# Kernel optimization log

Hardware: AMD Instinct MI355X
Metric: run time of the kernel (lower is better)

Reference implementation:

```python
import jax, jax.numpy as jnp
import numpy as np

NUM_HEADS = 8
DIM_IN = 512
DIM_OUT = 512


def setup_inputs() -> dict:
    key = jax.random.key(0)
    k1, k2, k3, k4, k5, k6 = jax.random.split(key, 6)
    B, T, J, C = 8, 243, 17, DIM_IN
    H = NUM_HEADS
    x = jax.random.normal(k1, (B, T, J, C), dtype=jnp.float32)
    # external attention map over temporal axis per joint: [B,H,J,T,T]
    att_map = jax.random.uniform(k2, (B, H, J, T, T), dtype=jnp.float32)
    weight = jax.random.uniform(k3, (1,), dtype=jnp.float32)
    # learned params (torch Linear stored here as [in,out] so y = x @ W)
    W_qkv = jax.random.normal(k4, (C, 3 * C), dtype=jnp.float32) * (C ** -0.5)
    W_proj = jax.random.normal(k5, (C, DIM_OUT), dtype=jnp.float32) * (C ** -0.5)
    b_proj = jax.random.normal(k6, (DIM_OUT,), dtype=jnp.float32) * 0.02
    return {"x": x, "att_map": att_map, "weight": weight,
            "W_qkv": W_qkv, "W_proj": W_proj, "b_proj": b_proj}


def reference(x, att_map, weight, W_qkv, W_proj, b_proj):
    B, T, J, C = x.shape
    H = NUM_HEADS
    hd = C // H
    scale = hd ** -0.5
    qkv = (x @ W_qkv).reshape(B, T, J, 3, H, hd)
    # permute(3,0,4,1,2,5) then transpose(2,3) -> [3,B,H,J,T,hd]
    qkv = jnp.transpose(qkv, (3, 0, 4, 2, 1, 5))
    q, k, v = qkv[0], qkv[1], qkv[2]
    attn = jax.nn.softmax(jnp.einsum('bhjtd,bhjsd->bhjts', q, k) * scale, axis=-1)
    attn = weight * attn + (1.0 - weight) * att_map  # dropout is identity (p=0 / eval)
    out = jnp.einsum('bhjts,bhjsd->bhjtd', attn, v)  # [B,H,J,T,hd]
    out = jnp.transpose(out, (0, 3, 2, 1, 4)).reshape(B, T, J, H * hd)
    return out @ W_proj + b_proj
```

## Files before the change

kernel.cpp:

```cpp
#include <hip/hip_runtime.h>
#include <cstddef>
#include <cstdint>

#define NHEADS 8
#define TT 243
#define JJ 17
#define BB 8
#define CC 512
#define HD 64
#define MROWS 33048
#define TJ 4131
#define HJ 136

typedef __attribute__((ext_vector_type(8))) short bf16x8;
typedef __attribute__((ext_vector_type(4))) float f32x4;

__device__ __forceinline__ unsigned short f2bf(float f) {
    unsigned u = __float_as_uint(f);
    unsigned r = (u + 0x7fff + ((u >> 16) & 1)) >> 16;
    return (unsigned short)r;
}
__device__ __forceinline__ float b2f(unsigned short u) {
    return __uint_as_float(((unsigned)u) << 16);
}
__device__ __forceinline__ void async16(const void* g, void* l) {
    __builtin_amdgcn_global_load_lds(
        (const __attribute__((address_space(1))) void*)g,
        (__attribute__((address_space(3))) void*)l, 16, 0, 0);
}

__global__ __launch_bounds__(256) void convert_x(
    const float* __restrict__ in, unsigned short* __restrict__ out, int n4)
{
    for (int i = blockIdx.x * 256 + threadIdx.x; i < n4; i += gridDim.x * 256) {
        const float4 v = *(const float4*)(in + (size_t)i * 4);
        ushort4 o;
        o.x = f2bf(v.x); o.y = f2bf(v.y); o.z = f2bf(v.z); o.w = f2bf(v.w);
        *(ushort4*)(out + (size_t)i * 4) = o;
    }
}

__global__ __launch_bounds__(256) void transpose_w(
    const float* __restrict__ src, unsigned short* __restrict__ dst, int N)
{
    __shared__ unsigned short tile[64][65];
    const int tid = threadIdx.x;
    const int c = tid & 63, r4 = tid >> 6;
    const int n0 = blockIdx.x << 6, k0 = blockIdx.y << 6;
    #pragma unroll
    for (int p = 0; p < 16; ++p) {
        const int r = (p << 2) + r4;
        tile[r][c] = f2bf(src[(size_t)(k0 + r) * N + n0 + c]);
    }
    __syncthreads();
    #pragma unroll
    for (int p = 0; p < 16; ++p) {
        const int rr = (p << 2) + r4;
        dst[(size_t)(n0 + rr) * 512 + k0 + c] = tile[c][rr];
    }
}

__global__ __launch_bounds__(256) void gemm_qkv(
    const unsigned short* __restrict__ xb, const unsigned short* __restrict__ wt,
    unsigned short* __restrict__ qb, unsigned short* __restrict__ kb,
    unsigned short* __restrict__ vb)
{
    __shared__ __align__(16) char smem[32768];
    char* const A0 = smem;
    char* const A1 = smem + 8192;
    char* const B0 = smem + 16384;
    char* const B1 = smem + 24576;

    const int tid = threadIdx.x;
    const int wave = tid >> 6, lane = tid & 63;
    const int m0 = blockIdx.y << 7, n0 = blockIdx.x << 7;
    const int wr = wave >> 1, wc = wave & 1;

    f32x4 acc[4][4];
    #pragma unroll
    for (int i = 0; i < 4; ++i)
        #pragma unroll
        for (int j = 0; j < 4; ++j) acc[i][j] = (f32x4){0.f, 0.f, 0.f, 0.f};

    const int srow = lane >> 2;
    const int sbyte = (lane & 3) << 4;
    const int arow0 = (wave << 5) + srow;
    const int arow1 = arow0 + 16;
    const size_t am0 = (size_t)min(m0 + arow0, MROWS - 1);
    const size_t am1 = (size_t)min(m0 + arow1, MROWS - 1);
    const char* xbb = (const char*)xb;
    const char* wtb = (const char*)wt;

#define STAGEQ(Ad, Bd, k0) do { \
    async16(xbb + (am0 * 512 + (k0)) * 2 + sbyte, (Ad) + ((wave << 5) << 6)); \
    async16(xbb + (am1 * 512 + (k0)) * 2 + sbyte, (Ad) + (((wave << 5) + 16) << 6)); \
    async16(wtb + ((size_t)(n0 + arow0) * 512 + (k0)) * 2 + sbyte, (Bd) + ((wave << 5) << 6)); \
    async16(wtb + ((size_t)(n0 + arow1) * 512 + (k0)) * 2 + sbyte, (Bd) + (((wave << 5) + 16) << 6)); \
} while (0)

#define COMPUTEQ(Ap, Bp) do { \
    bf16x8 af[4], bfr[4]; \
    _Pragma("unroll") \
    for (int i = 0; i < 4; ++i) \
        af[i] = *(const bf16x8*)((const unsigned short*)(Ap) + \
            ((wr << 6) + (i << 4) + (lane & 15)) * 32 + ((lane >> 4) << 3)); \
    _Pragma("unroll") \
    for (int j = 0; j < 4; ++j) \
        bfr[j] = *(const bf16x8*)((const unsigned short*)(Bp) + \
            ((wc << 6) + (j << 4) + (lane & 15)) * 32 + ((lane >> 4) << 3)); \
    _Pragma("unroll") \
    for (int i = 0; i < 4; ++i) \
        _Pragma("unroll") \
        for (int j = 0; j < 4; ++j) \
            acc[i][j] = __builtin_amdgcn_mfma_f32_16x16x32_bf16(af[i], bfr[j], acc[i][j], 0, 0, 0); \
} while (0)

    STAGEQ(A0, B0, 0);
    __syncthreads();
    #pragma unroll
    for (int t = 0; t < 16; t += 2) {
        STAGEQ(A1, B1, (t + 1) << 5);
        COMPUTEQ(A0, B0);
        __syncthreads();
        if (t + 2 < 16) STAGEQ(A0, B0, (t + 2) << 5);
        COMPUTEQ(A1, B1);
        __syncthreads();
    }
#undef STAGEQ
#undef COMPUTEQ

    unsigned short (*Cq)[16][72] = (unsigned short (*)[16][72])smem;

    const int nw = n0 + (wc << 6);
    const int which = nw >> 9;
    const int h = (nw >> 6) & 7;
    unsigned short* const dst = which == 0 ? qb : (which == 1 ? kb : vb);
    #pragma unroll
    for (int i = 0; i < 4; ++i) {
        #pragma unroll
        for (int j = 0; j < 4; ++j)
            #pragma unroll
            for (int r = 0; r < 4; ++r)
                Cq[wave][((lane >> 4) << 2) + r][(j << 4) + (lane & 15)] = f2bf(acc[i][j][r]);
        #pragma unroll
        for (int qq = 0; qq < 4; ++qq) {
            const int rr = (qq << 2) + (lane >> 4);
            const int ch = lane & 15;
            const ushort4 val = *(const ushort4*)&Cq[wave][rr][ch << 2];
            const int m = m0 + (wr << 6) + (i << 4) + rr;
            if (m < MROWS) {
                const int b = m / TJ; const int rm = m - b * TJ;
                const int t = rm / JJ; const int jj = rm - t * JJ;
                const size_t base = (((size_t)((b * NHEADS + h) * JJ + jj) * TT + t) << 6) + (ch << 2);
                *(ushort4*)(dst + base) = val;
            }
        }
    }
}

__global__ __launch_bounds__(256) void vtrans(
    const unsigned short* __restrict__ vb, unsigned short* __restrict__ vt)
{
    __shared__ unsigned short TL[64 * 264];
    const int tid = threadIdx.x;
    const int bhj = blockIdx.x;
    const unsigned short* src = vb + (size_t)bhj * TT * HD;

    {
        const int d = tid >> 2, qq = tid & 3;
        *(ushort4*)(TL + d * 264 + 240 + (qq << 2)) = make_ushort4(0, 0, 0, 0);
    }
    __syncthreads();
    #pragma unroll
    for (int p = 0; p < 16; ++p) {
        const int idxq = tid + (p << 8);
        const int t = idxq >> 4;
        if (t < TT) {
            const int d0 = (idxq & 15) << 2;
            const ushort4 u = *(const ushort4*)(src + t * HD + d0);
            TL[(d0 + 0) * 264 + t] = u.x;
            TL[(d0 + 1) * 264 + t] = u.y;
            TL[(d0 + 2) * 264 + t] = u.z;
            TL[(d0 + 3) * 264 + t] = u.w;
        }
    }
    __syncthreads();
    unsigned short* dst = vt + ((size_t)bhj << 14);
    #pragma unroll
    for (int p = 0; p < 8; ++p) {
        const int cw = tid + (p << 8);
        const int d = cw >> 5, c = cw & 31;
        const ushort4 a = *(const ushort4*)(TL + d * 264 + (c << 3));
        const ushort4 bq = *(const ushort4*)(TL + d * 264 + (c << 3) + 4);
        *(ushort4*)(dst + (d << 8) + (c << 3)) = a;
        *(ushort4*)(dst + (d << 8) + (c << 3) + 4) = bq;
    }
}

__global__ __launch_bounds__(256, 4) void attn_mfma(
    const unsigned short* __restrict__ qb, const unsigned short* __restrict__ kb,
    const unsigned short* __restrict__ vt, const float* __restrict__ att,
    const float* __restrict__ wptr, unsigned short* __restrict__ ob)
{
    __shared__ unsigned short ST[64 * 264];

    const int tid = threadIdx.x;
    const int wave = tid >> 6, lane = tid & 63;
    const int tile = blockIdx.x & 3, bhj = blockIdx.x >> 2;
    const int row0 = tile << 6;

    const unsigned short* q = qb + (size_t)bhj * TT * HD;
    const unsigned short* k = kb + (size_t)bhj * TT * HD;
    const float* am = att + (size_t)bhj * TT * TT;
    const float w = wptr[0];

    const int lm = lane & 15, lk = lane >> 4;
    bf16x8 qf[4][2];
    #pragma unroll
    for (int mi = 0; mi < 4; ++mi) {
        const int r = min(row0 + (mi << 4) + lm, TT - 1);
        #pragma unroll
        for (int kb2 = 0; kb2 < 2; ++kb2)
            qf[mi][kb2] = *(const bf16x8*)(q + r * HD + (kb2 << 5) + (lk << 3));
    }
    f32x4 acc[4][4];
    #pragma unroll
    for (int mi = 0; mi < 4; ++mi)
        #pragma unroll
        for (int nj = 0; nj < 4; ++nj) acc[mi][nj] = (f32x4){0.f, 0.f, 0.f, 0.f};
    #pragma unroll
    for (int kb2 = 0; kb2 < 2; ++kb2) {
        bf16x8 kf[4];
        #pragma unroll
        for (int nj = 0; nj < 4; ++nj) {
            const int s = min((wave << 6) + (nj << 4) + lm, TT - 1);
            kf[nj] = *(const bf16x8*)(k + s * HD + (kb2 << 5) + (lk << 3));
        }
        #pragma unroll
        for (int mi = 0; mi < 4; ++mi)
            #pragma unroll
            for (int nj = 0; nj < 4; ++nj)
                acc[mi][nj] = __builtin_amdgcn_mfma_f32_16x16x32_bf16(qf[mi][kb2], kf[nj], acc[mi][nj], 0, 0, 0);
    }
    #pragma unroll
    for (int mi = 0; mi < 4; ++mi)
        #pragma unroll
        for (int nj = 0; nj < 4; ++nj)
            #pragma unroll
            for (int r = 0; r < 4; ++r) {
                const int m = (mi << 4) + (lk << 2) + r;
                const int s = (wave << 6) + (nj << 4) + lm;
                ST[m * 264 + s] = f2bf(acc[mi][nj][r] * 0.125f);
            }
    __syncthreads();

    {
        const int row = tid >> 2, part = tid & 3;
        const int trow = row0 + row;
        unsigned short* strow = ST + row * 264;
        if (trow < TT) {
            const float* amr = am + (size_t)trow * TT;

            float areg[15][4];
            #pragma unroll
            for (int i = 0; i < 15; ++i) {
                const int s0 = (part << 2) + (i << 4);
                areg[i][0] = amr[s0 + 0];
                areg[i][1] = amr[s0 + 1];
                areg[i][2] = amr[s0 + 2];
                areg[i][3] = amr[s0 + 3];
            }
            float at0 = 0.f, at1 = 0.f, at2 = 0.f;
            if (part == 0) { at0 = amr[240]; at1 = amr[241]; at2 = amr[242]; }

            float mx = -1e30f;
            #pragma unroll
            for (int i = 0; i < 15; ++i) {
                const ushort4 u = *(const ushort4*)(strow + (part << 2) + (i << 4));
                mx = fmaxf(fmaxf(fmaxf(fmaxf(mx, b2f(u.x)), b2f(u.y)), b2f(u.z)), b2f(u.w));
            }
            if (part == 0)
                for (int s = 240; s < TT; ++s) mx = fmaxf(mx, b2f(strow[s]));
            mx = fmaxf(mx, __shfl_xor(mx, 1));
            mx = fmaxf(mx, __shfl_xor(mx, 2));
            float l = 0.f;
            #pragma unroll
            for (int i = 0; i < 15; ++i) {
                const int s0 = (part << 2) + (i << 4);
                const ushort4 u = *(const ushort4*)(strow + s0);
                const float e0 = __expf(b2f(u.x) - mx), e1 = __expf(b2f(u.y) - mx);
                const float e2 = __expf(b2f(u.z) - mx), e3 = __expf(b2f(u.w) - mx);
                l += (e0 + e1) + (e2 + e3);
                ushort4 o;
                o.x = f2bf(e0); o.y = f2bf(e1); o.z = f2bf(e2); o.w = f2bf(e3);
                *(ushort4*)(strow + s0) = o;
            }
            if (part == 0)
                for (int s = 240; s < TT; ++s) {
                    const float e = __expf(b2f(strow[s]) - mx);
                    l += e; strow[s] = f2bf(e);
                }
            l += __shfl_xor(l, 1);
            l += __shfl_xor(l, 2);
            const float sw = w / l, aw = 1.f - w;
            #pragma unroll
            for (int i = 0; i < 15; ++i) {
                const int s0 = (part << 2) + (i << 4);
                const ushort4 u = *(const ushort4*)(strow + s0);
                ushort4 o;
                o.x = f2bf(b2f(u.x) * sw + aw * areg[i][0]);
                o.y = f2bf(b2f(u.y) * sw + aw * areg[i][1]);
                o.z = f2bf(b2f(u.z) * sw + aw * areg[i][2]);
                o.w = f2bf(b2f(u.w) * sw + aw * areg[i][3]);
                *(ushort4*)(strow + s0) = o;
            }
            if (part == 0) {
                strow[240] = f2bf(b2f(strow[240]) * sw + aw * at0);
                strow[241] = f2bf(b2f(strow[241]) * sw + aw * at1);
                strow[242] = f2bf(b2f(strow[242]) * sw + aw * at2);
                for (int s = TT; s < 256; ++s) strow[s] = 0;
            }
        } else {
            #pragma unroll
            for (int i = 0; i < 16; ++i)
                *(ushort4*)(strow + (part << 2) + (i << 4)) = make_ushort4(0, 0, 0, 0);
        }
    }
    __syncthreads();

    f32x4 oacc[4];
    #pragma unroll
    for (int nj = 0; nj < 4; ++nj) oacc[nj] = (f32x4){0.f, 0.f, 0.f, 0.f};
    const unsigned short* strow3 = ST + ((wave << 4) + lm) * 264;
    const unsigned short* vtg = vt + ((size_t)bhj << 14);
    #pragma unroll 2
    for (int kb8 = 0; kb8 < 8; ++kb8) {
        const bf16x8 pf = *(const bf16x8*)(strow3 + (kb8 << 5) + (lk << 3));
        #pragma unroll
        for (int nj = 0; nj < 4; ++nj) {
            const int d = (nj << 4) + lm;
            const int chunk = (kb8 << 2) + lk;
            const bf16x8 vf = *(const bf16x8*)(vtg + (d << 8) + (chunk << 3));
            oacc[nj] = __builtin_amdgcn_mfma_f32_16x16x32_bf16(pf, vf, oacc[nj], 0, 0, 0);
        }
    }

    const int b = bhj / HJ;
    const int hj = bhj - b * HJ;
    const int h = hj / JJ;
    const int j = hj - h * JJ;
    #pragma unroll
    for (int r = 0; r < 4; ++r) {
        const int t = row0 + (wave << 4) + (lk << 2) + r;
        if (t < TT) {
            unsigned short* orow = ob + (((size_t)((b * TT + t) * JJ + j)) << 9) + (h << 6);
            #pragma unroll
            for (int nj = 0; nj < 4; ++nj)
                orow[(nj << 4) + lm] = f2bf(oacc[nj][r]);
        }
    }
}

__global__ __launch_bounds__(256) void gemm_proj(
    const unsigned short* __restrict__ obb, const unsigned short* __restrict__ wt,
    const float* __restrict__ bias, float* __restrict__ out)
{
    __shared__ __align__(16) char smem[32768];
    char* const A0 = smem;
    char* const A1 = smem + 8192;
    char* const B0 = smem + 16384;
    char* const B1 = smem + 24576;

    const int tid = threadIdx.x;
    const int wave = tid >> 6, lane = tid & 63;
    const int m0 = blockIdx.y << 7, n0 = blockIdx.x << 7;
    const int wr = wave >> 1, wc = wave & 1;

    f32x4 acc[4][4];
    #pragma unroll
    for (int i = 0; i < 4; ++i)
        #pragma unroll
        for (int j = 0; j < 4; ++j) acc[i][j] = (f32x4){0.f, 0.f, 0.f, 0.f};

    const int srow = lane >> 2;
    const int sbyte = (lane & 3) << 4;
    const int arow0 = (wave << 5) + srow;
    const int arow1 = arow0 + 16;
    const size_t am0 = (size_t)min(m0 + arow0, MROWS - 1);
    const size_t am1 = (size_t)min(m0 + arow1, MROWS - 1);
    const char* ab = (const char*)obb;
    const char* wtb = (const char*)wt;

#define STAGEP(Ad, Bd, k0) do { \
    async16(ab + (am0 * 512 + (k0)) * 2 + sbyte, (Ad) + ((wave << 5) << 6)); \
    async16(ab + (am1 * 512 + (k0)) * 2 + sbyte, (Ad) + (((wave << 5) + 16) << 6)); \
    async16(wtb + ((size_t)(n0 + arow0) * 512 + (k0)) * 2 + sbyte, (Bd) + ((wave << 5) << 6)); \
    async16(wtb + ((size_t)(n0 + arow1) * 512 + (k0)) * 2 + sbyte, (Bd) + (((wave << 5) + 16) << 6)); \
} while (0)

#define COMPUTEP(Ap, Bp) do { \
    bf16x8 af[4], bfr[4]; \
    _Pragma("unroll") \
    for (int i = 0; i < 4; ++i) \
        af[i] = *(const bf16x8*)((const unsigned short*)(Ap) + \
            ((wr << 6) + (i << 4) + (lane & 15)) * 32 + ((lane >> 4) << 3)); \
    _Pragma("unroll") \
    for (int j = 0; j < 4; ++j) \
        bfr[j] = *(const bf16x8*)((const unsigned short*)(Bp) + \
            ((wc << 6) + (j << 4) + (lane & 15)) * 32 + ((lane >> 4) << 3)); \
    _Pragma("unroll") \
    for (int i = 0; i < 4; ++i) \
        _Pragma("unroll") \
        for (int j = 0; j < 4; ++j) \
            acc[i][j] = __builtin_amdgcn_mfma_f32_16x16x32_bf16(af[i], bfr[j], acc[i][j], 0, 0, 0); \
} while (0)

    STAGEP(A0, B0, 0);
    __syncthreads();
    #pragma unroll
    for (int t = 0; t < 16; t += 2) {
        STAGEP(A1, B1, (t + 1) << 5);
        COMPUTEP(A0, B0);
        __syncthreads();
        if (t + 2 < 16) STAGEP(A0, B0, (t + 2) << 5);
        COMPUTEP(A1, B1);
        __syncthreads();
    }
#undef STAGEP
#undef COMPUTEP

    float (*Cp)[16][68] = (float (*)[16][68])smem;

    const int ch0 = lane & 15;
    const float4 bvec = *(const float4*)&bias[n0 + (wc << 6) + (ch0 << 2)];
    #pragma unroll
    for (int i = 0; i < 4; ++i) {
        #pragma unroll
        for (int j = 0; j < 4; ++j)
            #pragma unroll
            for (int r = 0; r < 4; ++r)
                Cp[wave][((lane >> 4) << 2) + r][(j << 4) + (lane & 15)] = acc[i][j][r];
        #pragma unroll
        for (int qq = 0; qq < 4; ++qq) {
            const int rr = (qq << 2) + (lane >> 4);
            const int ch = lane & 15;
            float4 val = *(const float4*)&Cp[wave][rr][ch << 2];
            const int m = m0 + (wr << 6) + (i << 4) + rr;
            if (m < MROWS) {
                val.x += bvec.x; val.y += bvec.y; val.z += bvec.z; val.w += bvec.w;
                *(float4*)(out + (size_t)m * 512 + n0 + (wc << 6) + (ch << 2)) = val;
            }
        }
    }
}

extern "C" void kernel_launch(void* const* d_in, const int* in_sizes, int n_in,
                              void* d_out, int out_size, void* d_ws, size_t ws_size,
                              hipStream_t stream)
{
    const float* x    = (const float*)d_in[0];
    const float* att  = (const float*)d_in[1];
    const float* wgt  = (const float*)d_in[2];
    const float* Wqkv = (const float*)d_in[3];
    const float* Wp   = (const float*)d_in[4];
    const float* bp   = (const float*)d_in[5];
    float* out = (float*)d_out;

    const size_t SZ = (size_t)MROWS * 512;
    unsigned short* xb    = (unsigned short*)d_ws;
    unsigned short* wqkvt = xb + SZ;
    unsigned short* wpt   = wqkvt + (size_t)1536 * 512;
    unsigned short* qb    = wpt + (size_t)512 * 512;
    unsigned short* kb    = qb + SZ;
    unsigned short* vb    = kb + SZ;
    unsigned short* ob    = vb + SZ;
    unsigned short* vtb   = ob + SZ;

    convert_x<<<4096, 256, 0, stream>>>(x, xb, (int)(SZ / 4));
    transpose_w<<<dim3(24, 8), 256, 0, stream>>>(Wqkv, wqkvt, 1536);
    transpose_w<<<dim3(8, 8), 256, 0, stream>>>(Wp, wpt, 512);

    gemm_qkv<<<dim3(12, 259), 256, 0, stream>>>(xb, wqkvt, qb, kb, vb);

    vtrans<<<dim3(1088), 256, 0, stream>>>(vb, vtb);

    attn_mfma<<<dim3(1088 * 4), 256, 0, stream>>>(qb, kb, vtb, att, wgt, ob);

    gemm_proj<<<dim3(4, 259), 256, 0, stream>>>(ob, wpt, bp, out);
}
```

Before: 600.1 us.

## Prefetch attention-map rows before QK MFMA and keep softmax exponentials in registers

The attention-map rows are now loaded with vectorized 16-byte loads before the QK^T MFMA loop, so their global latency overlaps the matrix math instead of sitting after the barrier. The softmax exponentials stay in fp32 registers rather than being rounded to bf16 and written back to LDS before the blend pass. All K fragments are also loaded up front, and f2bf now uses the HIP intrinsic. To make room for the extra registers, launch_bounds drops from 4 to 2 blocks per SM, which lowers occupancy in exchange for more overlap.

Result: no change. 593.8 us (-1.0%).

```diff
diff --git a/kernel.cpp b/kernel.cpp
--- a/kernel.cpp
+++ b/kernel.cpp
@@ -1,4 +1,5 @@
 #include <hip/hip_runtime.h>
+#include <hip/hip_bf16.h>
 #include <cstddef>
 #include <cstdint>
 
@@ -14,11 +15,10 @@
 
 typedef __attribute__((ext_vector_type(8))) short bf16x8;
 typedef __attribute__((ext_vector_type(4))) float f32x4;
+typedef __attribute__((ext_vector_type(4), aligned(4))) float f32x4u;
 
 __device__ __forceinline__ unsigned short f2bf(float f) {
-    unsigned u = __float_as_uint(f);
-    unsigned r = (u + 0x7fff + ((u >> 16) & 1)) >> 16;
-    return (unsigned short)r;
+    return __builtin_bit_cast(unsigned short, __float2bfloat16(f));
 }
 __device__ __forceinline__ float b2f(unsigned short u) {
     return __uint_as_float(((unsigned)u) << 16);
@@ -197,7 +197,7 @@
     }
 }
 
-__global__ __launch_bounds__(256, 4) void attn_mfma(
+__global__ __launch_bounds__(256, 2) void attn_mfma(
     const unsigned short* __restrict__ qb, const unsigned short* __restrict__ kb,
     const unsigned short* __restrict__ vt, const float* __restrict__ att,
     const float* __restrict__ wptr, unsigned short* __restrict__ ob)
@@ -215,6 +215,7 @@
     const float w = wptr[0];
 
     const int lm = lane & 15, lk = lane >> 4;
+
     bf16x8 qf[4][2];
     #pragma unroll
     for (int mi = 0; mi < 4; ++mi) {
@@ -223,25 +224,39 @@
         for (int kb2 = 0; kb2 < 2; ++kb2)
             qf[mi][kb2] = *(const bf16x8*)(q + r * HD + (kb2 << 5) + (lk << 3));
     }
-    f32x4 acc[4][4];
-    #pragma unroll
-    for (int mi = 0; mi < 4; ++mi)
-        #pragma unroll
-        for (int nj = 0; nj < 4; ++nj) acc[mi][nj] = (f32x4){0.f, 0.f, 0.f, 0.f};
-    #pragma unroll
-    for (int kb2 = 0; kb2 < 2; ++kb2) {
-        bf16x8 kf[4];
+    bf16x8 kf[2][4];
+    #pragma unroll
+    for (int kb2 = 0; kb2 < 2; ++kb2)
         #pragma unroll
         for (int nj = 0; nj < 4; ++nj) {
             const int s = min((wave << 6) + (nj << 4) + lm, TT - 1);
-            kf[nj] = *(const bf16x8*)(k + s * HD + (kb2 << 5) + (lk << 3));
-        }
+            kf[kb2][nj] = *(const bf16x8*)(k + s * HD + (kb2 << 5) + (lk << 3));
+        }
+
+    const int row2 = tid >> 2, part = tid & 3;
+    const int trow2 = row0 + row2;
+    const float* amr = am + (size_t)min(trow2, TT - 1) * TT;
+    float areg[15][4];
+    #pragma unroll
+    for (int i = 0; i < 15; ++i) {
+        const f32x4u av = *(const f32x4u*)(amr + (part << 2) + (i << 4));
+        areg[i][0] = av.x; areg[i][1] = av.y; areg[i][2] = av.z; areg[i][3] = av.w;
+    }
+    float at0 = 0.f, at1 = 0.f, at2 = 0.f;
+    if (part == 0) { at0 = amr[240]; at1 = amr[241]; at2 = amr[242]; }
+
+    f32x4 acc[4][4];
+    #pragma unroll
+    for (int mi = 0; mi < 4; ++mi)
+        #pragma unroll
+        for (int nj = 0; nj < 4; ++nj) acc[mi][nj] = (f32x4){0.f, 0.f, 0.f, 0.f};
+    #pragma unroll
+    for (int kb2 = 0; kb2 < 2; ++kb2)
         #pragma unroll
         for (int mi = 0; mi < 4; ++mi)
             #pragma unroll
             for (int nj = 0; nj < 4; ++nj)
-                acc[mi][nj] = __builtin_amdgcn_mfma_f32_16x16x32_bf16(qf[mi][kb2], kf[nj], acc[mi][nj], 0, 0, 0);
-    }
+                acc[mi][nj] = __builtin_amdgcn_mfma_f32_16x16x32_bf16(qf[mi][kb2], kf[kb2][nj], acc[mi][nj], 0, 0, 0);
     #pragma unroll
     for (int mi = 0; mi < 4; ++mi)
         #pragma unroll
@@ -255,24 +270,8 @@
     __syncthreads();
 
     {
-        const int row = tid >> 2, part = tid & 3;
-        const int trow = row0 + row;
-        unsigned short* strow = ST + row * 264;
-        if (trow < TT) {
-            const float* amr = am + (size_t)trow * TT;
-
-            float areg[15][4];
-            #pragma unroll
-            for (int i = 0; i < 15; ++i) {
-                const int s0 = (part << 2) + (i << 4);
-                areg[i][0] = amr[s0 + 0];
-                areg[i][1] = amr[s0 + 1];
-                areg[i][2] = amr[s0 + 2];
-                areg[i][3] = amr[s0 + 3];
-            }
-            float at0 = 0.f, at1 = 0.f, at2 = 0.f;
-            if (part == 0) { at0 = amr[240]; at1 = amr[241]; at2 = amr[242]; }
-
+        unsigned short* strow = ST + row2 * 264;
+        if (trow2 < TT) {
             float mx = -1e30f;
             #pragma unroll
             for (int i = 0; i < 15; ++i) {
@@ -283,41 +282,43 @@
                 for (int s = 240; s < TT; ++s) mx = fmaxf(mx, b2f(strow[s]));
             mx = fmaxf(mx, __shfl_xor(mx, 1));
             mx = fmaxf(mx, __shfl_xor(mx, 2));
+
+            float er[15][4];
             float l = 0.f;
             #pragma unroll
             for (int i = 0; i < 15; ++i) {
                 const int s0 = (part << 2) + (i << 4);
                 const ushort4 u = *(const ushort4*)(strow + s0);
-                const float e0 = __expf(b2f(u.x) - mx), e1 = __expf(b2f(u.y) - mx);
-                const float e2 = __expf(b2f(u.z) - mx), e3 = __expf(b2f(u.w) - mx);
-                l += (e0 + e1) + (e2 + e3);
-                ushort4 o;
-                o.x = f2bf(e0); o.y = f2bf(e1); o.z = f2bf(e2); o.w = f2bf(e3);
-                *(ushort4*)(strow + s0) = o;
-            }
-            if (part == 0)
-                for (int s = 240; s < TT; ++s) {
-                    const float e = __expf(b2f(strow[s]) - mx);
-                    l += e; strow[s] = f2bf(e);
-                }
+                er[i][0] = __expf(b2f(u.x) - mx);
+                er[i][1] = __expf(b2f(u.y) - mx);
+                er[i][2] = __expf(b2f(u.z) - mx);
+                er[i][3] = __expf(b2f(u.w) - mx);
+                l += (er[i][0] + er[i][1]) + (er[i][2] + er[i][3]);
+            }
+            float et0 = 0.f, et1 = 0.f, et2 = 0.f;
+            if (part == 0) {
+                et0 = __expf(b2f(strow[240]) - mx);
+                et1 = __expf(b2f(strow[241]) - mx);
+                et2 = __expf(b2f(strow[242]) - mx);
+                l += et0 + et1 + et2;
+            }
             l += __shfl_xor(l, 1);
             l += __shfl_xor(l, 2);
             const float sw = w / l, aw = 1.f - w;
             #pragma unroll
             for (int i = 0; i < 15; ++i) {
                 const int s0 = (part << 2) + (i << 4);
-                const ushort4 u = *(const ushort4*)(strow + s0);
                 ushort4 o;
-                o.x = f2bf(b2f(u.x) * sw + aw * areg[i][0]);
-                o.y = f2bf(b2f(u.y) * sw + aw * areg[i][1]);
-                o.z = f2bf(b2f(u.z) * sw + aw * areg[i][2]);
-                o.w = f2bf(b2f(u.w) * sw + aw * areg[i][3]);
+                o.x = f2bf(er[i][0] * sw + aw * areg[i][0]);
+                o.y = f2bf(er[i][1] * sw + aw * areg[i][1]);
+                o.z = f2bf(er[i][2] * sw + aw * areg[i][2]);
+                o.w = f2bf(er[i][3] * sw + aw * areg[i][3]);
                 *(ushort4*)(strow + s0) = o;
             }
             if (part == 0) {
-                strow[240] = f2bf(b2f(strow[240]) * sw + aw * at0);
-                strow[241] = f2bf(b2f(strow[241]) * sw + aw * at1);
-                strow[242] = f2bf(b2f(strow[242]) * sw + aw * at2);
+                strow[240] = f2bf(et0 * sw + aw * at0);
+                strow[241] = f2bf(et1 * sw + aw * at1);
+                strow[242] = f2bf(et2 * sw + aw * at2);
                 for (int s = TT; s < 256; ++s) strow[s] = 0;
             }
         } else {
```
